# Kernel optimization log

Measured on AMD Instinct MI355X. Metric: run time of the kernel, lower is better.

The kernel has to match this reference:

```python
import jax, jax.numpy as jnp
import numpy as np

D_MODEL = 2048
N_HEADS = 16
D_HEAD = D_MODEL // N_HEADS


def setup_inputs() -> dict:
    key = jax.random.key(0)
    k1, k2, k3, k4, k5 = jax.random.split(key, 5)
    x = jax.random.normal(k1, (4, 2048, D_MODEL), dtype=jnp.float32)
    s = 1.0 / np.sqrt(D_MODEL)
    qkv_w = jax.random.normal(k2, (3 * D_MODEL, D_MODEL), dtype=jnp.float32) * s
    qkv_b = jax.random.normal(k3, (3 * D_MODEL,), dtype=jnp.float32) * 0.01
    out_w = jax.random.normal(k4, (D_MODEL, D_MODEL), dtype=jnp.float32) * s
    out_b = jax.random.normal(k5, (D_MODEL,), dtype=jnp.float32) * 0.01
    return {"x": x, "qkv_w": qkv_w, "qkv_b": qkv_b, "out_w": out_w, "out_b": out_b}


def reference(x, qkv_w, qkv_b, out_w, out_b):
    B, T, D = x.shape
    # fused QKV projection: (B,T,D) -> (B,T,3D), torch Linear uses W^T
    qkv = jnp.einsum('btd,ed->bte', x, qkv_w) + qkv_b
    qkv = qkv.reshape(B, T, 3, N_HEADS, D_HEAD)
    qkv = jnp.transpose(qkv, (2, 0, 3, 1, 4))  # (3, B, H, T, Dh)
    q, k, v = qkv[0], qkv[1], qkv[2]
    # scaled dot-product attention (non-causal)
    scale = 1.0 / jnp.sqrt(jnp.asarray(D_HEAD, dtype=x.dtype))
    scores = jnp.einsum('bhqd,bhkd->bhqk', q, k) * scale
    attn = jax.nn.softmax(scores, axis=-1)
    out = jnp.einsum('bhqk,bhkd->bhqd', attn, v)
    out = jnp.transpose(out, (0, 2, 1, 3)).reshape(B, T, D)
    return jnp.einsum('btd,ed->bte', out, out_w) + out_b
```

## Files before the change

### kernel.cpp

```cpp
#include <hip/hip_runtime.h>

typedef unsigned short u16;
typedef __attribute__((ext_vector_type(8))) __bf16 bf16x8;
typedef __attribute__((ext_vector_type(4))) float f32x4;

#define SEQ 2048
#define DMODEL 2048
#define NHEADS 16
#define DHEAD 128

typedef __attribute__((address_space(1))) void gvoid_t;
typedef __attribute__((address_space(3))) void lvoid_t;

__device__ inline void gload_lds16(const void* g, void* l) {
  __builtin_amdgcn_global_load_lds((gvoid_t*)g, (lvoid_t*)l, 16, 0, 0);
}

__device__ inline u16 f2bf(float f) {
  unsigned u = __float_as_uint(f);
  unsigned r = (u + 0x7fffu + ((u >> 16) & 1u)) >> 16;
  return (u16)r;
}

__global__ __launch_bounds__(256) void cvt_f32_bf16(const float* __restrict__ in,
                                                    u16* __restrict__ out, int n4) {
  int i = blockIdx.x * 256 + threadIdx.x;
  if (i >= n4) return;
  float4 v = reinterpret_cast<const float4*>(in)[i];
  ushort4 o;
  o.x = f2bf(v.x); o.y = f2bf(v.y); o.z = f2bf(v.z); o.w = f2bf(v.w);
  reinterpret_cast<ushort4*>(out)[i] = o;
}

#define GBAR() __builtin_amdgcn_s_barrier()
#define SB0() __builtin_amdgcn_sched_barrier(0)
#define WAITLGKM(N) do { asm volatile("s_waitcnt lgkmcnt(" #N ")" ::: "memory"); } while (0)
#define WAITVM(N) do { asm volatile("s_waitcnt vmcnt(" #N ")" ::: "memory"); } while (0)

template <int MODE>
__global__ __launch_bounds__(512, 1) void gemm256(
    const u16* __restrict__ A, const u16* __restrict__ B,
    const float* __restrict__ bias, int M, int N, int K, int nby,
    u16* __restrict__ qb, u16* __restrict__ kb, u16* __restrict__ vtb,
    float* __restrict__ outf) {
  __shared__ __align__(16) u16 As[2][256 * 64];
  __shared__ __align__(16) u16 Bs[2][256 * 64];
  const int nwg = gridDim.x;
  const int cpx = nwg >> 3;
  const int bid = blockIdx.x;
  const int sw = (bid & 7) * cpx + (bid >> 3);
  const int bx = sw / nby, by = sw % nby;
  const int m0 = bx * 256, n0 = by * 256;
  const int tid = threadIdx.x, lane = tid & 63, w = tid >> 6;
  const int wm = w >> 2, wn = w & 3;
  const int fr = lane & 15, hi = lane >> 4;
  const int g4 = hi * 4;
  const u16* Abase = A + (size_t)m0 * K;
  const u16* Bbase = B + (size_t)n0 * K;

  f32x4 acc[8][4];
#pragma unroll
  for (int i = 0; i < 8; i++)
#pragma unroll
    for (int j = 0; j < 4; j++) acc[i][j] = f32x4{0.f, 0.f, 0.f, 0.f};

#define STAGE(T, P)                                                              \
  do {                                                                           \
    const int t64 = (T) * 64;                                                    \
    _Pragma("unroll") for (int j = 0; j < 4; j++) {                              \
      const int U = (j * 8 + w) * 64 + lane;                                     \
      const int r_ = U >> 3;                                                     \
      const int us = (lane & 7) ^ (r_ & 7);                                      \
      gload_lds16(Abase + (size_t)r_ * K + t64 + us * 8, &As[P][U * 8]);         \
      gload_lds16(Bbase + (size_t)r_ * K + t64 + us * 8, &Bs[P][U * 8]);         \
    }                                                                            \
  } while (0)

#define LDA(AF, H, P)                                                            \
  do {                                                                           \
    _Pragma("unroll") for (int fi = 0; fi < 4; fi++) {                           \
      const int row = wm * 128 + (H) * 64 + fi * 16 + fr;                        \
      _Pragma("unroll") for (int kk = 0; kk < 2; kk++) {                         \
        const int u = (kk * 4 + hi) ^ (row & 7);                                 \
        AF[fi][kk] = *(const bf16x8*)&As[P][row * 64 + u * 8];                    \
      }                                                                          \
    }                                                                            \
  } while (0)

#define LDB(BF, G, P)                                                            \
  do {                                                                           \
    _Pragma("unroll") for (int fj = 0; fj < 2; fj++) {                           \
      const int row = wn * 64 + (G) * 32 + fj * 16 + fr;                         \
      _Pragma("unroll") for (int kk = 0; kk < 2; kk++) {                         \
        const int u = (kk * 4 + hi) ^ (row & 7);                                 \
        BF[fj][kk] = *(const bf16x8*)&Bs[P][row * 64 + u * 8];                    \
      }                                                                          \
    }                                                                            \
  } while (0)

#define MF(AF, BF, H, G)                                                         \
  do {                                                                           \
    __builtin_amdgcn_s_setprio(1);                                               \
    _Pragma("unroll") for (int kk = 0; kk < 2; kk++)                             \
    _Pragma("unroll") for (int fi = 0; fi < 4; fi++)                             \
    _Pragma("unroll") for (int fj = 0; fj < 2; fj++)                             \
      acc[(H) * 4 + fi][(G) * 2 + fj] = __builtin_amdgcn_mfma_f32_16x16x32_bf16( \
          AF[fi][kk], BF[fj][kk], acc[(H) * 4 + fi][(G) * 2 + fj], 0, 0, 0);     \
    __builtin_amdgcn_s_setprio(0);                                               \
  } while (0)

#define TILE(T, P)                                                               \
  do {                                                                           \
    LDA(a, 0, P); SB0();                                                         \
    LDB(b0, 0, P); SB0();                                                        \
    LDB(b1, 1, P); SB0();                                                        \
    GBAR(); SB0();                                                               \
    WAITLGKM(4); SB0();                                                          \
    MF(a, b0, 0, 0);                                                             \
    WAITLGKM(0); SB0();                                                          \
    MF(a, b1, 0, 1);                                                             \
    LDA(a, 1, P); SB0();                                                         \
    WAITLGKM(0); SB0();                                                          \
    GBAR(); SB0();                                                               \
    if ((T) + 2 < NT) STAGE((T) + 2, P);                                         \
    SB0();                                                                       \
    MF(a, b0, 1, 0);                                                             \
    MF(a, b1, 1, 1);                                                             \
    if ((T) + 2 < NT) { WAITVM(8); }                                             \
    else if ((T) + 1 < NT) { WAITVM(0); }                                        \
    SB0();                                                                       \
    GBAR(); SB0();                                                               \
  } while (0)

  const int NT = K >> 6;
  STAGE(0, 0);
  STAGE(1, 1);
  WAITVM(8); SB0();
  GBAR(); SB0();

  bf16x8 a[4][2], b0[2][2], b1[2][2];
  for (int t = 0; t + 1 < NT; t += 2) {
    TILE(t, 0);
    TILE(t + 1, 1);
  }

  if (MODE == 0) {
    const int which = n0 >> 11;
#pragma unroll
    for (int mi = 0; mi < 8; mi++) {
      const int trow = m0 + wm * 128 + mi * 16 + g4;
      const int b = trow >> 11;
      const int t = trow & 2047;
#pragma unroll
      for (int nj = 0; nj < 4; nj++) {
        const int col = n0 + wn * 64 + nj * 16 + fr;
        const int h = (col >> 7) & 15;
        const int dh = col & 127;
        const float bv = bias[col];
        if (which == 2) {
          ushort4 pk;
          pk.x = f2bf(acc[mi][nj][0] + bv);
          pk.y = f2bf(acc[mi][nj][1] + bv);
          pk.z = f2bf(acc[mi][nj][2] + bv);
          pk.w = f2bf(acc[mi][nj][3] + bv);
          *reinterpret_cast<ushort4*>(vtb + ((size_t)(b * NHEADS + h) * DHEAD + dh) * SEQ + t) = pk;
        } else {
          u16* dst = (which == 0) ? qb : kb;
          const float sc = (which == 0) ? 0.08838834764831845f : 1.0f;
#pragma unroll
          for (int r = 0; r < 4; r++)
            dst[((size_t)(b * NHEADS + h) * SEQ + (t + r)) * DHEAD + dh] =
                f2bf((acc[mi][nj][r] + bv) * sc);
        }
      }
    }
  } else {
#pragma unroll
    for (int mi = 0; mi < 8; mi++) {
      const int row = m0 + wm * 128 + mi * 16 + g4;
#pragma unroll
      for (int nj = 0; nj < 4; nj++) {
        const int col = n0 + wn * 64 + nj * 16 + fr;
        const float bv = bias[col];
#pragma unroll
        for (int r = 0; r < 4; r++) outf[(size_t)(row + r) * N + col] = acc[mi][nj][r] + bv;
      }
    }
  }
#undef STAGE
#undef LDA
#undef LDB
#undef MF
#undef TILE
}

__global__ __launch_bounds__(256, 2) void attn_fwd(const u16* __restrict__ Q,
                                                   const u16* __restrict__ Kb,
                                                   const u16* __restrict__ VT,
                                                   u16* __restrict__ O) {
  __shared__ __align__(16) u16 Ks[64 * 128];
  __shared__ __align__(16) u16 Vs[128 * 64];
  __shared__ __align__(16) u16 P_lds[4][32][72];
  const int bh = blockIdx.y;
  const int b = bh >> 4, h = bh & 15;
  const int w = threadIdx.x >> 6;
  const int lane = threadIdx.x & 63;
  const int fr = lane & 15;
  const int hi = lane >> 4;
  const int kr = hi * 8;
  const int g4 = hi * 4;
  const int q0w = blockIdx.x * 128 + w * 32;

  const u16* Qp = Q + (size_t)bh * SEQ * DHEAD;
  const u16* Kp = Kb + (size_t)bh * SEQ * DHEAD;
  const u16* Vp = VT + (size_t)bh * DHEAD * SEQ;

  bf16x8 qf[2][4];
#pragma unroll
  for (int mg = 0; mg < 2; mg++)
#pragma unroll
    for (int kk = 0; kk < 4; kk++)
      qf[mg][kk] = *(const bf16x8*)(Qp + (size_t)(q0w + mg * 16 + fr) * DHEAD + kk * 32 + kr);

  f32x4 oacc[2][8];
#pragma unroll
  for (int mg = 0; mg < 2; mg++)
#pragma unroll
    for (int i = 0; i < 8; i++) oacc[mg][i] = f32x4{0.f, 0.f, 0.f, 0.f};
  float mrun[2] = {-1e30f, -1e30f};
  float lrun[2] = {0.f, 0.f};

  bf16x8 kreg[4], vreg[4];
#pragma unroll
  for (int i = 0; i < 4; i++) {
    const int u = w * 256 + i * 64 + lane;
    const int rK = u >> 4, c16 = u & 15;
    kreg[i] = *(const bf16x8*)(Kp + (size_t)rK * DHEAD + c16 * 8);
    const int rV = u >> 3, c8 = u & 7;
    vreg[i] = *(const bf16x8*)(Vp + (size_t)rV * SEQ + c8 * 8);
  }

  for (int kv0 = 0; kv0 < SEQ; kv0 += 64) {
    __syncthreads();
#pragma unroll
    for (int i = 0; i < 4; i++) {
      const int u = w * 256 + i * 64 + lane;
      const int rK = u >> 4, c16 = u & 15;
      *(bf16x8*)&Ks[rK * 128 + ((c16 ^ (rK & 7)) * 8)] = kreg[i];
      const int rV = u >> 3, c8 = u & 7;
      *(bf16x8*)&Vs[rV * 64 + ((c8 ^ (rV & 7)) * 8)] = vreg[i];
    }
    __syncthreads();
    if (kv0 + 64 < SEQ) {
      const int kvn = kv0 + 64;
#pragma unroll
      for (int i = 0; i < 4; i++) {
        const int u = w * 256 + i * 64 + lane;
        const int rK = u >> 4, c16 = u & 15;
        kreg[i] = *(const bf16x8*)(Kp + (size_t)(kvn + rK) * DHEAD + c16 * 8);
        const int rV = u >> 3, c8 = u & 7;
        vreg[i] = *(const bf16x8*)(Vp + (size_t)rV * SEQ + kvn + c8 * 8);
      }
    }

    f32x4 s[2][4];
#pragma unroll
    for (int mg = 0; mg < 2; mg++)
#pragma unroll
      for (int ct = 0; ct < 4; ct++) s[mg][ct] = f32x4{0.f, 0.f, 0.f, 0.f};
    __builtin_amdgcn_s_setprio(1);
#pragma unroll
    for (int kk = 0; kk < 4; kk++) {
#pragma unroll
      for (int ct = 0; ct < 4; ct++) {
        const int row = ct * 16 + fr;
        bf16x8 kf = *(const bf16x8*)&Ks[row * 128 + (((kk * 4 + hi) ^ (row & 7)) * 8)];
        s[0][ct] = __builtin_amdgcn_mfma_f32_16x16x32_bf16(kf, qf[0][kk], s[0][ct], 0, 0, 0);
        s[1][ct] = __builtin_amdgcn_mfma_f32_16x16x32_bf16(kf, qf[1][kk], s[1][ct], 0, 0, 0);
      }
    }
    __builtin_amdgcn_s_setprio(0);

    float pm[2];
#pragma unroll
    for (int mg = 0; mg < 2; mg++) {
      f32x4 mv = s[mg][0];
      mv[0] = fmaxf(mv[0], s[mg][1][0]); mv[1] = fmaxf(mv[1], s[mg][1][1]);
      mv[2] = fmaxf(mv[2], s[mg][1][2]); mv[3] = fmaxf(mv[3], s[mg][1][3]);
      mv[0] = fmaxf(mv[0], s[mg][2][0]); mv[1] = fmaxf(mv[1], s[mg][2][1]);
      mv[2] = fmaxf(mv[2], s[mg][2][2]); mv[3] = fmaxf(mv[3], s[mg][2][3]);
      mv[0] = fmaxf(mv[0], s[mg][3][0]); mv[1] = fmaxf(mv[1], s[mg][3][1]);
      mv[2] = fmaxf(mv[2], s[mg][3][2]); mv[3] = fmaxf(mv[3], s[mg][3][3]);
      float p = fmaxf(fmaxf(mv[0], mv[1]), fmaxf(mv[2], mv[3]));
      p = fmaxf(p, __shfl_xor(p, 16, 64));
      p = fmaxf(p, __shfl_xor(p, 32, 64));
      pm[mg] = p;
    }

    const bool need = (pm[0] - mrun[0] > 8.f) || (pm[1] - mrun[1] > 8.f);
    if (__any(need)) {
#pragma unroll
      for (int mg = 0; mg < 2; mg++) {
        float nm = fmaxf(mrun[mg], pm[mg]);
        float sfv = __expf(mrun[mg] - nm);
        mrun[mg] = nm;
        lrun[mg] *= sfv;
        float fac[4];
#pragma unroll
        for (int r = 0; r < 4; r++) fac[r] = __shfl(sfv, g4 + r, 64);
#pragma unroll
        for (int dt = 0; dt < 8; dt++) {
          oacc[mg][dt][0] *= fac[0]; oacc[mg][dt][1] *= fac[1];
          oacc[mg][dt][2] *= fac[2]; oacc[mg][dt][3] *= fac[3];
        }
      }
    }

#pragma unroll
    for (int mg = 0; mg < 2; mg++) {
#pragma unroll
      for (int ct = 0; ct < 4; ct++)
#pragma unroll
        for (int r = 0; r < 4; r++) s[mg][ct][r] = __expf(s[mg][ct][r] - mrun[mg]);
      f32x4 sv = s[mg][0] + s[mg][1] + s[mg][2] + s[mg][3];
      float su = (sv[0] + sv[1]) + (sv[2] + sv[3]);
      su += __shfl_xor(su, 16, 64);
      su += __shfl_xor(su, 32, 64);
      lrun[mg] += su;
#pragma unroll
      for (int ct = 0; ct < 4; ct++) {
        ushort4 pk;
        pk.x = f2bf(s[mg][ct][0]); pk.y = f2bf(s[mg][ct][1]);
        pk.z = f2bf(s[mg][ct][2]); pk.w = f2bf(s[mg][ct][3]);
        *reinterpret_cast<ushort4*>(&P_lds[w][mg * 16 + fr][ct * 16 + g4]) = pk;
      }
    }

    bf16x8 pf[2][2];
#pragma unroll
    for (int mg = 0; mg < 2; mg++)
#pragma unroll
      for (int kk = 0; kk < 2; kk++)
        pf[mg][kk] = *(const bf16x8*)&P_lds[w][mg * 16 + fr][kk * 32 + kr];
    __builtin_amdgcn_s_setprio(1);
#pragma unroll
    for (int kk = 0; kk < 2; kk++) {
#pragma unroll
      for (int dt = 0; dt < 8; dt++) {
        const int row = dt * 16 + fr;
        bf16x8 vf = *(const bf16x8*)&Vs[row * 64 + (((kk * 4 + hi) ^ (row & 7)) * 8)];
        oacc[0][dt] = __builtin_amdgcn_mfma_f32_16x16x32_bf16(pf[0][kk], vf, oacc[0][dt], 0, 0, 0);
        oacc[1][dt] = __builtin_amdgcn_mfma_f32_16x16x32_bf16(pf[1][kk], vf, oacc[1][dt], 0, 0, 0);
      }
    }
    __builtin_amdgcn_s_setprio(0);
  }

#pragma unroll
  for (int mg = 0; mg < 2; mg++) {
    float linv = 1.0f / lrun[mg];
    float fac[4];
#pragma unroll
    for (int r = 0; r < 4; r++) fac[r] = __shfl(linv, g4 + r, 64);
#pragma unroll
    for (int r = 0; r < 4; r++) {
      const int t = q0w + mg * 16 + g4 + r;
      u16* op = O + ((size_t)(b * SEQ + t)) * DMODEL + h * DHEAD;
#pragma unroll
      for (int dt = 0; dt < 8; dt++) op[dt * 16 + fr] = f2bf(oacc[mg][dt][r] * fac[r]);
    }
  }
}

extern "C" void kernel_launch(void* const* d_in, const int* in_sizes, int n_in,
                              void* d_out, int out_size, void* d_ws, size_t ws_size,
                              hipStream_t stream) {
  const float* x = (const float*)d_in[0];
  const float* qkv_w = (const float*)d_in[1];
  const float* qkv_b = (const float*)d_in[2];
  const float* out_w = (const float*)d_in[3];
  const float* out_b = (const float*)d_in[4];
  float* out = (float*)d_out;

  char* ws = (char*)d_ws;
  u16* xb = (u16*)ws;
  u16* wqkv = (u16*)(ws + 33554432);
  u16* qb = (u16*)(ws + 33554432 + 25165824);
  u16* kb = qb + (size_t)64 * SEQ * DHEAD;
  u16* vtb = kb + (size_t)64 * SEQ * DHEAD;
  u16* attnb = xb;
  u16* outwb = wqkv;

  cvt_f32_bf16<<<16777216 / 4 / 256, 256, 0, stream>>>(x, xb, 16777216 / 4);
  cvt_f32_bf16<<<12582912 / 4 / 256, 256, 0, stream>>>(qkv_w, wqkv, 12582912 / 4);
  gemm256<0><<<768, 512, 0, stream>>>(xb, wqkv, qkv_b, 8192, 6144, 2048, 24, qb, kb, vtb,
                                      nullptr);
  cvt_f32_bf16<<<4194304 / 4 / 256, 256, 0, stream>>>(out_w, outwb, 4194304 / 4);
  dim3 ga(SEQ / 128, 64);
  attn_fwd<<<ga, 256, 0, stream>>>(qb, kb, vtb, attnb);
  gemm256<1><<<256, 512, 0, stream>>>(attnb, outwb, out_b, 8192, 2048, 2048, 8, nullptr,
                                      nullptr, nullptr, out);
}
```

Measured before the change: 479.9 us.

## Split GEMM tile prefetch into per-quarter loads interleaved with MFMA phases

The next-tile global-to-LDS stage is broken into individual A and B slices. Each slice is issued as soon as the LDS region it overwrites has been consumed, spread across the four MFMA phases of a tile instead of one burst in the middle. Each phase now waits for all LDS reads and hits a barrier before its MFMAs. The aim is to overlap global memory traffic more evenly with matrix math in the QKV and output projection GEMMs. The cost is more workgroup barriers per tile, and correctness relies on the row partitioning lining up with which fragments have already been read.

```diff
diff --git a/kernel.cpp b/kernel.cpp
--- a/kernel.cpp
+++ b/kernel.cpp
@@ -64,16 +64,19 @@
 #pragma unroll
     for (int j = 0; j < 4; j++) acc[i][j] = f32x4{0.f, 0.f, 0.f, 0.f};
 
-#define STAGE(T, P)                                                              \
-  do {                                                                           \
-    const int t64 = (T) * 64;                                                    \
-    _Pragma("unroll") for (int j = 0; j < 4; j++) {                              \
-      const int U = (j * 8 + w) * 64 + lane;                                     \
-      const int r_ = U >> 3;                                                     \
-      const int us = (lane & 7) ^ (r_ & 7);                                      \
-      gload_lds16(Abase + (size_t)r_ * K + t64 + us * 8, &As[P][U * 8]);         \
-      gload_lds16(Bbase + (size_t)r_ * K + t64 + us * 8, &Bs[P][U * 8]);         \
-    }                                                                            \
+#define STAGE_A1(T, P, J)                                                        \
+  do {                                                                           \
+    const int U = ((J) * 8 + w) * 64 + lane;                                     \
+    const int r_ = U >> 3;                                                       \
+    const int us = (lane & 7) ^ (r_ & 7);                                        \
+    gload_lds16(Abase + (size_t)r_ * K + (T) * 64 + us * 8, &As[P][U * 8]);      \
+  } while (0)
+#define STAGE_B1(T, P, J)                                                        \
+  do {                                                                           \
+    const int U = ((J) * 8 + w) * 64 + lane;                                     \
+    const int r_ = U >> 3;                                                       \
+    const int us = (lane & 7) ^ (r_ & 7);                                        \
+    gload_lds16(Bbase + (size_t)r_ * K + (T) * 64 + us * 8, &Bs[P][U * 8]);      \
   } while (0)
 
 #define LDA(AF, H, P)                                                            \
@@ -111,30 +114,43 @@
 
 #define TILE(T, P)                                                               \
   do {                                                                           \
-    LDA(a, 0, P); SB0();                                                         \
-    LDB(b0, 0, P); SB0();                                                        \
+                                                                        \
+    LDA(a, 0, P); LDB(b0, 0, P); SB0();                                          \
+    GBAR(); WAITLGKM(0); SB0();                                                  \
+    MF(a, b0, 0, 0);                                                             \
+    GBAR();                                                                      \
+                                                                        \
     LDB(b1, 1, P); SB0();                                                        \
-    GBAR(); SB0();                                                               \
-    WAITLGKM(4); SB0();                                                          \
-    MF(a, b0, 0, 0);                                                             \
-    WAITLGKM(0); SB0();                                                          \
+    if ((T) + 2 < NT) { STAGE_A1((T) + 2, P, 0); STAGE_A1((T) + 2, P, 2); }      \
+    SB0();                                                                       \
+    GBAR(); WAITLGKM(0); SB0();                                                  \
     MF(a, b1, 0, 1);                                                             \
+    GBAR();                                                                      \
+                                                                        \
     LDA(a, 1, P); SB0();                                                         \
-    WAITLGKM(0); SB0();                                                          \
-    GBAR(); SB0();                                                               \
-    if ((T) + 2 < NT) STAGE((T) + 2, P);                                         \
+    if ((T) + 2 < NT) { STAGE_B1((T) + 2, P, 0); STAGE_B1((T) + 2, P, 1); }      \
     SB0();                                                                       \
+    GBAR(); WAITLGKM(0); SB0();                                                  \
     MF(a, b0, 1, 0);                                                             \
+    GBAR();                                                                      \
+                                                                        \
+    if ((T) + 2 < NT) {                                                          \
+      STAGE_A1((T) + 2, P, 1); STAGE_A1((T) + 2, P, 3);                          \
+      STAGE_B1((T) + 2, P, 2); STAGE_B1((T) + 2, P, 3);                          \
+    }                                                                            \
+    SB0();                                                                       \
     MF(a, b1, 1, 1);                                                             \
     if ((T) + 2 < NT) { WAITVM(8); }                                             \
     else if ((T) + 1 < NT) { WAITVM(0); }                                        \
     SB0();                                                                       \
-    GBAR(); SB0();                                                               \
+    GBAR();                                                                      \
   } while (0)
 
   const int NT = K >> 6;
-  STAGE(0, 0);
-  STAGE(1, 1);
+#pragma unroll
+  for (int j = 0; j < 4; j++) { STAGE_A1(0, 0, j); STAGE_B1(0, 0, j); }
+#pragma unroll
+  for (int j = 0; j < 4; j++) { STAGE_A1(1, 1, j); STAGE_B1(1, 1, j); }
   WAITVM(8); SB0();
   GBAR(); SB0();
 
@@ -187,7 +203,8 @@
       }
     }
   }
-#undef STAGE
+#undef STAGE_A1
+#undef STAGE_B1
 #undef LDA
 #undef LDB
 #undef MF
```

New measurement: 479.7 us. Within noise of the previous version (-0.0%).

## Load V fragments directly from global into registers, dropping the V LDS stage

Applied to the files above, without the earlier changes.

The attention kernel no longer stages transposed V tiles through shared memory. Each wave loads its V MFMA fragments straight from global memory in two halves, one before the QK^T step and one before PV, with sched_barriers to keep the loads in place. This removes the V LDS writes and reads and frees LDS, but every wave now fetches the full V tile from global/L2 (4x redundant across waves), adds register pressure, and issues less-coalesced strided loads. The GEMM MFMA loop order is also reordered so kk is the innermost loop.

```diff
diff --git a/kernel.cpp b/kernel.cpp
--- a/kernel.cpp
+++ b/kernel.cpp
@@ -101,9 +101,9 @@
 #define MF(AF, BF, H, G)                                                         \
   do {                                                                           \
     __builtin_amdgcn_s_setprio(1);                                               \
-    _Pragma("unroll") for (int kk = 0; kk < 2; kk++)                             \
     _Pragma("unroll") for (int fi = 0; fi < 4; fi++)                             \
     _Pragma("unroll") for (int fj = 0; fj < 2; fj++)                             \
+    _Pragma("unroll") for (int kk = 0; kk < 2; kk++)                             \
       acc[(H) * 4 + fi][(G) * 2 + fj] = __builtin_amdgcn_mfma_f32_16x16x32_bf16( \
           AF[fi][kk], BF[fj][kk], acc[(H) * 4 + fi][(G) * 2 + fj], 0, 0, 0);     \
     __builtin_amdgcn_s_setprio(0);                                               \
@@ -199,7 +199,6 @@
                                                    const u16* __restrict__ VT,
                                                    u16* __restrict__ O) {
   __shared__ __align__(16) u16 Ks[64 * 128];
-  __shared__ __align__(16) u16 Vs[128 * 64];
   __shared__ __align__(16) u16 P_lds[4][32][72];
   const int bh = blockIdx.y;
   const int b = bh >> 4, h = bh & 15;
@@ -230,14 +229,12 @@
   float mrun[2] = {-1e30f, -1e30f};
   float lrun[2] = {0.f, 0.f};
 
-  bf16x8 kreg[4], vreg[4];
+  bf16x8 kreg[4];
 #pragma unroll
   for (int i = 0; i < 4; i++) {
     const int u = w * 256 + i * 64 + lane;
     const int rK = u >> 4, c16 = u & 15;
     kreg[i] = *(const bf16x8*)(Kp + (size_t)rK * DHEAD + c16 * 8);
-    const int rV = u >> 3, c8 = u & 7;
-    vreg[i] = *(const bf16x8*)(Vp + (size_t)rV * SEQ + c8 * 8);
   }
 
   for (int kv0 = 0; kv0 < SEQ; kv0 += 64) {
@@ -247,10 +244,16 @@
       const int u = w * 256 + i * 64 + lane;
       const int rK = u >> 4, c16 = u & 15;
       *(bf16x8*)&Ks[rK * 128 + ((c16 ^ (rK & 7)) * 8)] = kreg[i];
-      const int rV = u >> 3, c8 = u & 7;
-      *(bf16x8*)&Vs[rV * 64 + ((c8 ^ (rV & 7)) * 8)] = vreg[i];
     }
     __syncthreads();
+
+    bf16x8 vfA[4][2], vfB[4][2];
+#pragma unroll
+    for (int dt = 0; dt < 4; dt++)
+#pragma unroll
+      for (int kk = 0; kk < 2; kk++)
+        vfA[dt][kk] = *(const bf16x8*)(Vp + (size_t)(dt * 16 + fr) * SEQ + kv0 + kk * 32 + kr);
+    __builtin_amdgcn_sched_barrier(0);
     if (kv0 + 64 < SEQ) {
       const int kvn = kv0 + 64;
 #pragma unroll
@@ -258,10 +261,9 @@
         const int u = w * 256 + i * 64 + lane;
         const int rK = u >> 4, c16 = u & 15;
         kreg[i] = *(const bf16x8*)(Kp + (size_t)(kvn + rK) * DHEAD + c16 * 8);
-        const int rV = u >> 3, c8 = u & 7;
-        vreg[i] = *(const bf16x8*)(Vp + (size_t)rV * SEQ + kvn + c8 * 8);
-      }
-    }
+      }
+    }
+    __builtin_amdgcn_sched_barrier(0);
 
     f32x4 s[2][4];
 #pragma unroll
@@ -336,21 +338,36 @@
       }
     }
 
+#pragma unroll
+    for (int dt = 0; dt < 4; dt++)
+#pragma unroll
+      for (int kk = 0; kk < 2; kk++)
+        vfB[dt][kk] =
+            *(const bf16x8*)(Vp + (size_t)((dt + 4) * 16 + fr) * SEQ + kv0 + kk * 32 + kr);
+    __builtin_amdgcn_sched_barrier(0);
+
     bf16x8 pf[2][2];
 #pragma unroll
     for (int mg = 0; mg < 2; mg++)
 #pragma unroll
       for (int kk = 0; kk < 2; kk++)
         pf[mg][kk] = *(const bf16x8*)&P_lds[w][mg * 16 + fr][kk * 32 + kr];
+
     __builtin_amdgcn_s_setprio(1);
 #pragma unroll
     for (int kk = 0; kk < 2; kk++) {
 #pragma unroll
-      for (int dt = 0; dt < 8; dt++) {
-        const int row = dt * 16 + fr;
-        bf16x8 vf = *(const bf16x8*)&Vs[row * 64 + (((kk * 4 + hi) ^ (row & 7)) * 8)];
-        oacc[0][dt] = __builtin_amdgcn_mfma_f32_16x16x32_bf16(pf[0][kk], vf, oacc[0][dt], 0, 0, 0);
-        oacc[1][dt] = __builtin_amdgcn_mfma_f32_16x16x32_bf16(pf[1][kk], vf, oacc[1][dt], 0, 0, 0);
+      for (int dt = 0; dt < 4; dt++) {
+        oacc[0][dt] = __builtin_amdgcn_mfma_f32_16x16x32_bf16(pf[0][kk], vfA[dt][kk], oacc[0][dt], 0, 0, 0);
+        oacc[1][dt] = __builtin_amdgcn_mfma_f32_16x16x32_bf16(pf[1][kk], vfA[dt][kk], oacc[1][dt], 0, 0, 0);
+      }
+    }
+#pragma unroll
+    for (int kk = 0; kk < 2; kk++) {
+#pragma unroll
+      for (int dt = 0; dt < 4; dt++) {
+        oacc[0][dt + 4] = __builtin_amdgcn_mfma_f32_16x16x32_bf16(pf[0][kk], vfB[dt][kk], oacc[0][dt + 4], 0, 0, 0);
+        oacc[1][dt + 4] = __builtin_amdgcn_mfma_f32_16x16x32_bf16(pf[1][kk], vfB[dt][kk], oacc[1][dt + 4], 0, 0, 0);
       }
     }
     __builtin_amdgcn_s_setprio(0);
```

New measurement: 540.5 us. +12.6%, slower.
